# Kernel tuning notes

Measured on AMD Instinct MI355X. Metric: run time of the kernel, lower is better.

Reference implementation:

```python
import jax, jax.numpy as jnp
import numpy as np

SQRT_QKV_DIM = 8.0  # sqrt(qkv_dim=64)


def setup_inputs() -> dict:
    key = jax.random.key(0)
    ks = jax.random.split(key, 8)
    B, H, T, M, d, hid = 4, 16, 512, 512, 64, 16
    return {
        "q": jax.random.normal(ks[0], (B, H, T, d), dtype=jnp.float32),
        "k": jax.random.normal(ks[1], (B, H, M, d), dtype=jnp.float32),
        "v": jax.random.normal(ks[2], (B, H, M, d), dtype=jnp.float32),
        "D_TM": jax.random.uniform(ks[3], (B, T, M), dtype=jnp.float32),
        "mix1_weight": jax.random.uniform(ks[4], (H, 2, hid), minval=-0.7071, maxval=0.7071, dtype=jnp.float32),
        "mix1_bias": jax.random.uniform(ks[5], (H, hid), minval=-0.7071, maxval=0.7071, dtype=jnp.float32),
        "mix2_weight": jax.random.uniform(ks[6], (H, hid, 1), minval=-0.25, maxval=0.25, dtype=jnp.float32),
        "mix2_bias": jax.random.uniform(ks[7], (H, 1), minval=-0.25, maxval=0.25, dtype=jnp.float32),
    }


def reference(q, k, v, D_TM, mix1_weight, mix1_bias, mix2_weight, mix2_bias):
    B, H, T, d = q.shape
    Mc = k.shape[2]
    # scaled dot-product score: (B,H,T,M)
    dot_score = jnp.einsum("bhtd,bhmd->bhtm", q, k) / SQRT_QKV_DIM
    # per-head 2->hidden->1 MLP mixing dot score and distance bias.
    # Avoid explicit stack: linear layer over the 2 score channels expands as
    # dot*W1[:,0,:] + D*W1[:,1,:].  ms1: (B,H,T,M,hid)
    w1_dot = mix1_weight[:, 0, :][None, :, None, None, :]   # (1,H,1,1,hid)
    w1_dist = mix1_weight[:, 1, :][None, :, None, None, :]
    ms1 = (dot_score[..., None] * w1_dot
           + D_TM[:, None, :, :, None] * w1_dist
           + mix1_bias[None, :, None, None, :])
    ms1 = jax.nn.relu(ms1)
    # hidden -> 1: mixed_scores (B,H,T,M)
    mixed = jnp.einsum("bhtmc,hc->bhtm", ms1, mix2_weight[:, :, 0])
    mixed = mixed + mix2_bias[:, 0][None, :, None, None]
    weights = jax.nn.softmax(mixed, axis=3)
    out = jnp.einsum("bhtm,bhmd->bhtd", weights, v)   # (B,H,T,d)
    return out.transpose(0, 2, 1, 3).reshape(B, T, H * d)
```

## Files before the change

### kernel.cpp

```cpp
#include <hip/hip_runtime.h>
#include <stdint.h>

typedef __attribute__((ext_vector_type(8))) short short8;
typedef __attribute__((ext_vector_type(4))) float floatx4;

#define MFMA(a, b, c) __builtin_amdgcn_mfma_f32_16x16x32_bf16(a, b, c, 0, 0, 0)

union Frag { uint32_t u[4]; short8 s; };

__device__ __forceinline__ void packsplit(float a, float b, uint32_t& hi, uint32_t& lo) {
    uint32_t ua = __float_as_uint(a), ub = __float_as_uint(b);
    uint32_t ha = ua & 0xFFFF0000u, hb = ub & 0xFFFF0000u;
    float ra = a - __uint_as_float(ha);
    float rb = b - __uint_as_float(hb);
    hi = (ha >> 16) | hb;
    lo = (__float_as_uint(ra) >> 16) | (__float_as_uint(rb) & 0xFFFF0000u);
}

#define KHI 0
#define KLO 4608
#define VTHI 0
#define VTLO 4352
#define PHI 8704
#define PLO 13056

__global__ __launch_bounds__(256, 2)
void msmha_mfma(const float* __restrict__ qg, const float* __restrict__ kg,
                const float* __restrict__ vg, const float* __restrict__ Dg,
                const float* __restrict__ m1w, const float* __restrict__ m1b,
                const float* __restrict__ m2w, const float* __restrict__ m2b,
                float* __restrict__ outg) {
    __shared__ __align__(16) uint32_t sm[17408];
    __shared__ __align__(16) float wlds[68];

    const int tid  = threadIdx.x;
    const int w    = tid >> 6;
    const int lane = tid & 63;
    const int col  = lane & 15;
    const int quad = lane >> 4;

    const int bid = blockIdx.x;
    const int wgT = bid & 7;
    const int bh  = bid >> 3;
    const int h   = bh & 15;
    const int b   = bh >> 4;
    const int t0g = wgT * 64;

    const size_t base = (size_t)bh * 512 * 64;

    if (tid < 16) {
        wlds[4 * tid + 0] = m1w[h * 32 + tid];
        wlds[4 * tid + 1] = m1w[h * 32 + 16 + tid];
        wlds[4 * tid + 2] = m1b[h * 16 + tid];
        wlds[4 * tid + 3] = m2w[h * 16 + tid];
    }
    if (tid == 16) wlds[64] = m2b[h];

    Frag qh[2], ql[2];
    {
        const float* qrow = qg + base + (size_t)(t0g + w * 16 + col) * 64;
#pragma unroll
        for (int ks = 0; ks < 2; ++ks) {
            const float4 f0 = *(const float4*)(qrow + ks * 32 + quad * 8);
            const float4 f1 = *(const float4*)(qrow + ks * 32 + quad * 8 + 4);
            packsplit(f0.x, f0.y, qh[ks].u[0], ql[ks].u[0]);
            packsplit(f0.z, f0.w, qh[ks].u[1], ql[ks].u[1]);
            packsplit(f1.x, f1.y, qh[ks].u[2], ql[ks].u[2]);
            packsplit(f1.z, f1.w, qh[ks].u[3], ql[ks].u[3]);
        }
    }

    floatx4 accA[32];

    const float* Dbase = Dg + ((size_t)b * 512 + t0g + w * 16 + col) * 512 + quad * 4;

#pragma unroll
    for (int mc = 0; mc < 4; ++mc) {
        __syncthreads();
#pragma unroll
        for (int it = 0; it < 8; ++it) {
            const int i  = tid + it * 256;
            const int ml = i >> 4, k4 = i & 15;
            const float4 f = *(const float4*)(kg + base + (size_t)(mc * 128 + ml) * 64 + k4 * 4);
            uint32_t h0, l0, h1, l1;
            packsplit(f.x, f.y, h0, l0);
            packsplit(f.z, f.w, h1, l1);
            *(uint2*)(sm + KHI + ml * 36 + 2 * k4) = make_uint2(h0, h1);
            *(uint2*)(sm + KLO + ml * 36 + 2 * k4) = make_uint2(l0, l1);
        }
        __syncthreads();

        float4 dv[8];
#pragma unroll
        for (int mt = 0; mt < 8; ++mt)
            dv[mt] = *(const float4*)(Dbase + mc * 128 + mt * 16);

#pragma unroll
        for (int mt = 0; mt < 8; ++mt) {
            floatx4 acc = {0.f, 0.f, 0.f, 0.f};
#pragma unroll
            for (int ks = 0; ks < 2; ++ks) {
                const int ro = (mt * 16 + col) * 36 + 16 * ks + 4 * quad;
                Frag ah, al;
                ah.s = *(short8*)(sm + KHI + ro);
                al.s = *(short8*)(sm + KLO + ro);
                acc = MFMA(ah.s, qh[ks].s, acc);
                acc = MFMA(ah.s, ql[ks].s, acc);
                acc = MFMA(al.s, qh[ks].s, acc);
            }
            accA[mc * 8 + mt] = acc;
        }

        float mix[32];
        const float b2v = wlds[64];
#pragma unroll
        for (int mt = 0; mt < 8; ++mt)
#pragma unroll
            for (int r = 0; r < 4; ++r) {
                accA[mc * 8 + mt][r] *= 0.125f;
                mix[mt * 4 + r] = b2v;
            }
#pragma unroll 1
        for (int c = 0; c < 16; ++c) {
            const float4 wv = *(const float4*)(wlds + 4 * c);
#pragma unroll
            for (int mt = 0; mt < 8; ++mt) {
                const float4 dd = dv[mt];
                const float dr[4] = {dd.x, dd.y, dd.z, dd.w};
#pragma unroll
                for (int r = 0; r < 4; ++r) {
                    const float hh = fmaf(accA[mc * 8 + mt][r], wv.x, fmaf(dr[r], wv.y, wv.z));
                    mix[mt * 4 + r] = fmaf(fmaxf(hh, 0.f), wv.w, mix[mt * 4 + r]);
                }
            }
        }
#pragma unroll
        for (int mt = 0; mt < 8; ++mt)
#pragma unroll
            for (int r = 0; r < 4; ++r)
                accA[mc * 8 + mt][r] = mix[mt * 4 + r];
    }

    float mx = -3.4e38f;
#pragma unroll
    for (int i = 0; i < 32; ++i)
#pragma unroll
        for (int r = 0; r < 4; ++r) mx = fmaxf(mx, accA[i][r]);
    mx = fmaxf(mx, __shfl_xor(mx, 16, 64));
    mx = fmaxf(mx, __shfl_xor(mx, 32, 64));
    float sum = 0.f;
#pragma unroll
    for (int i = 0; i < 32; ++i)
#pragma unroll
        for (int r = 0; r < 4; ++r) {
            const float e = __expf(accA[i][r] - mx);
            accA[i][r] = e;
            sum += e;
        }
    sum += __shfl_xor(sum, 16, 64);
    sum += __shfl_xor(sum, 32, 64);
    const float rinv = 1.f / sum;
#pragma unroll
    for (int i = 0; i < 32; ++i)
#pragma unroll
        for (int r = 0; r < 4; ++r) accA[i][r] *= rinv;

    floatx4 oacc[4];
#pragma unroll
    for (int dt = 0; dt < 4; ++dt) oacc[dt] = floatx4{0.f, 0.f, 0.f, 0.f};

#pragma unroll
    for (int mc = 0; mc < 4; ++mc) {
        __syncthreads();
#pragma unroll
        for (int it = 0; it < 4; ++it) {
            const int u  = tid + it * 256;
            const int d4 = u & 15, m2 = u >> 4;
            const float4 f0 = *(const float4*)(vg + base + (size_t)(mc * 128 + 2 * m2) * 64 + d4 * 4);
            const float4 f1 = *(const float4*)(vg + base + (size_t)(mc * 128 + 2 * m2 + 1) * 64 + d4 * 4);
            const float a0[4] = {f0.x, f0.y, f0.z, f0.w};
            const float a1[4] = {f1.x, f1.y, f1.z, f1.w};
#pragma unroll
            for (int i = 0; i < 4; ++i) {
                uint32_t hw, lw;
                packsplit(a0[i], a1[i], hw, lw);
                sm[VTHI + (d4 * 4 + i) * 68 + m2] = hw;
                sm[VTLO + (d4 * 4 + i) * 68 + m2] = lw;
            }
        }
        {
            const int prow = (w * 16 + col) * 68;
#pragma unroll
            for (int mt = 0; mt < 8; ++mt) {
                const floatx4 pv = accA[mc * 8 + mt];
                uint32_t h0, l0, h1, l1;
                packsplit(pv[0], pv[1], h0, l0);
                packsplit(pv[2], pv[3], h1, l1);
                *(uint2*)(sm + PHI + prow + mt * 8 + 2 * quad) = make_uint2(h0, h1);
                *(uint2*)(sm + PLO + prow + mt * 8 + 2 * quad) = make_uint2(l0, l1);
            }
        }
        __syncthreads();
#pragma unroll
        for (int ks = 0; ks < 4; ++ks) {
            const int po = (w * 16 + col) * 68 + 16 * ks + 4 * quad;
            Frag pah, pal;
            pah.s = *(short8*)(sm + PHI + po);
            pal.s = *(short8*)(sm + PLO + po);
#pragma unroll
            for (int dt = 0; dt < 4; ++dt) {
                const int vo = (dt * 16 + col) * 68 + 16 * ks + 4 * quad;
                Frag bh, bl;
                bh.s = *(short8*)(sm + VTHI + vo);
                bl.s = *(short8*)(sm + VTLO + vo);
                oacc[dt] = MFMA(pah.s, bh.s, oacc[dt]);
                oacc[dt] = MFMA(pah.s, bl.s, oacc[dt]);
                oacc[dt] = MFMA(pal.s, bh.s, oacc[dt]);
            }
        }
    }

    const size_t obase = ((size_t)b * 512 + t0g + w * 16 + quad * 4) * 1024 + h * 64 + col;
#pragma unroll
    for (int dt = 0; dt < 4; ++dt)
#pragma unroll
        for (int r = 0; r < 4; ++r)
            outg[obase + (size_t)r * 1024 + dt * 16] = oacc[dt][r];
}

extern "C" void kernel_launch(void* const* d_in, const int* in_sizes, int n_in,
                              void* d_out, int out_size, void* d_ws, size_t ws_size,
                              hipStream_t stream) {
    const float* q   = (const float*)d_in[0];
    const float* k   = (const float*)d_in[1];
    const float* v   = (const float*)d_in[2];
    const float* dtm = (const float*)d_in[3];
    const float* m1w = (const float*)d_in[4];
    const float* m1b = (const float*)d_in[5];
    const float* m2w = (const float*)d_in[6];
    const float* m2b = (const float*)d_in[7];
    float* out = (float*)d_out;

    dim3 grid(4 * 16 * 8);
    dim3 block(256);
    msmha_mfma<<<grid, block, 0, stream>>>(q, k, v, dtm, m1w, m1b, m2w, m2b, out);
}
```

Before: 132.6 us.

## Double-buffer K/V loads, pack MLP with v_pk_fma, shuffle P fragments

Rewrites the kernel around 64-row K and V chunks held in double-buffered LDS, prefetching the next chunk into registers while computing the current one. The per-element MLP now runs on packed two-wide f32 FMAs. The P operand for the PV MFMA is rearranged with lane shuffles instead of a round trip through LDS. Smaller changes: the 1/8 scale is folded into Q, bf16 splitting now uses round-to-nearest, and a fourth lo*lo MFMA is added to QK. These cut LDS footprint and barrier stalls at the cost of extra shuffles, extra MFMAs and more synchronisation points.

```diff
diff --git a/kernel.cpp b/kernel.cpp
--- a/kernel.cpp
+++ b/kernel.cpp
@@ -1,231 +1,296 @@
 #include <hip/hip_runtime.h>
 #include <stdint.h>
 
+typedef __attribute__((ext_vector_type(2))) float fx2;
+typedef __attribute__((ext_vector_type(4))) float fx4;
 typedef __attribute__((ext_vector_type(8))) short short8;
-typedef __attribute__((ext_vector_type(4))) float floatx4;
-
-#define MFMA(a, b, c) __builtin_amdgcn_mfma_f32_16x16x32_bf16(a, b, c, 0, 0, 0)
+
+#define MFMA(a,b,c) __builtin_amdgcn_mfma_f32_16x16x32_bf16(a,b,c,0,0,0)
 
 union Frag { uint32_t u[4]; short8 s; };
 
+__device__ __forceinline__ uint32_t bf16rne(float x) {
+    uint32_t u = __float_as_uint(x);
+    return (u + 0x7FFFu + ((u >> 16) & 1u)) & 0xFFFF0000u;
+}
+
 __device__ __forceinline__ void packsplit(float a, float b, uint32_t& hi, uint32_t& lo) {
-    uint32_t ua = __float_as_uint(a), ub = __float_as_uint(b);
-    uint32_t ha = ua & 0xFFFF0000u, hb = ub & 0xFFFF0000u;
+    uint32_t ha = bf16rne(a), hb = bf16rne(b);
     float ra = a - __uint_as_float(ha);
     float rb = b - __uint_as_float(hb);
-    hi = (ha >> 16) | hb;
-    lo = (__float_as_uint(ra) >> 16) | (__float_as_uint(rb) & 0xFFFF0000u);
-}
-
-#define KHI 0
-#define KLO 4608
-#define VTHI 0
-#define VTLO 4352
-#define PHI 8704
-#define PLO 13056
+    hi = (ha >> 16) | (hb & 0xFFFF0000u);
+    lo = (bf16rne(ra) >> 16) | (bf16rne(rb) & 0xFFFF0000u);
+}
+
+__device__ __forceinline__ fx2 pkfma_bLO(fx2 a, fx2 b, fx2 c) {
+    fx2 d; asm("v_pk_fma_f32 %0, %1, %2, %3 op_sel:[0,0,0] op_sel_hi:[1,0,1]"
+               : "=v"(d) : "v"(a), "v"(b), "v"(c)); return d;
+}
+__device__ __forceinline__ fx2 pkfma_bHI(fx2 a, fx2 b, fx2 c) {
+    fx2 d; asm("v_pk_fma_f32 %0, %1, %2, %3 op_sel:[0,1,0] op_sel_hi:[1,1,1]"
+               : "=v"(d) : "v"(a), "v"(b), "v"(c)); return d;
+}
+__device__ __forceinline__ fx2 pkfma_bHI_cLO(fx2 a, fx2 b, fx2 c) {
+    fx2 d; asm("v_pk_fma_f32 %0, %1, %2, %3 op_sel:[0,1,0] op_sel_hi:[1,1,0]"
+               : "=v"(d) : "v"(a), "v"(b), "v"(c)); return d;
+}
 
 __global__ __launch_bounds__(256, 2)
-void msmha_mfma(const float* __restrict__ qg, const float* __restrict__ kg,
-                const float* __restrict__ vg, const float* __restrict__ Dg,
-                const float* __restrict__ m1w, const float* __restrict__ m1b,
-                const float* __restrict__ m2w, const float* __restrict__ m2b,
-                float* __restrict__ outg) {
-    __shared__ __align__(16) uint32_t sm[17408];
-    __shared__ __align__(16) float wlds[68];
+void msmha_v5(const float* __restrict__ qg, const float* __restrict__ kg,
+              const float* __restrict__ vg, const float* __restrict__ Dg,
+              const float* __restrict__ m1w, const float* __restrict__ m1b,
+              const float* __restrict__ m2w, const float* __restrict__ m2b,
+              float* __restrict__ outg) {
+    __shared__ __align__(16) uint32_t sm[9284];
+    float* smF = (float*)sm;
 
     const int tid  = threadIdx.x;
-    const int w    = tid >> 6;
-    const int lane = tid & 63;
-    const int col  = lane & 15;
-    const int quad = lane >> 4;
-
-    const int bid = blockIdx.x;
-    const int wgT = bid & 7;
-    const int bh  = bid >> 3;
-    const int h   = bh & 15;
-    const int b   = bh >> 4;
-    const int t0g = wgT * 64;
+    const int w    = tid >> 6, lane = tid & 63;
+    const int col  = lane & 15, Q = lane >> 4;
+
+    const int bid  = blockIdx.x;
+    const int tile = bid & 7, bh = bid >> 3;
+    const int h    = bh & 15, b = bh >> 4;
+    const int t0g  = tile * 64;
 
     const size_t base = (size_t)bh * 512 * 64;
 
     if (tid < 16) {
-        wlds[4 * tid + 0] = m1w[h * 32 + tid];
-        wlds[4 * tid + 1] = m1w[h * 32 + 16 + tid];
-        wlds[4 * tid + 2] = m1b[h * 16 + tid];
-        wlds[4 * tid + 3] = m2w[h * 16 + tid];
-    }
-    if (tid == 16) wlds[64] = m2b[h];
-
+        smF[9216 + 4*tid + 0] = m1w[h*32 + tid];
+        smF[9216 + 4*tid + 1] = m1w[h*32 + 16 + tid];
+        smF[9216 + 4*tid + 2] = m1b[h*16 + tid];
+        smF[9216 + 4*tid + 3] = m2w[h*16 + tid];
+    }
+    const float b2v = m2b[h];
+
+    const int trow = t0g + w*16 + col;
     Frag qh[2], ql[2];
     {
-        const float* qrow = qg + base + (size_t)(t0g + w * 16 + col) * 64;
+        const float* qr = qg + base + (size_t)trow * 64;
 #pragma unroll
         for (int ks = 0; ks < 2; ++ks) {
-            const float4 f0 = *(const float4*)(qrow + ks * 32 + quad * 8);
-            const float4 f1 = *(const float4*)(qrow + ks * 32 + quad * 8 + 4);
+            fx4 f0 = *(const fx4*)(qr + ks*32 + Q*8);
+            fx4 f1 = *(const fx4*)(qr + ks*32 + Q*8 + 4);
+            f0 *= 0.125f; f1 *= 0.125f;
             packsplit(f0.x, f0.y, qh[ks].u[0], ql[ks].u[0]);
             packsplit(f0.z, f0.w, qh[ks].u[1], ql[ks].u[1]);
             packsplit(f1.x, f1.y, qh[ks].u[2], ql[ks].u[2]);
             packsplit(f1.z, f1.w, qh[ks].u[3], ql[ks].u[3]);
         }
     }
-
-    floatx4 accA[32];
-
-    const float* Dbase = Dg + ((size_t)b * 512 + t0g + w * 16 + col) * 512 + quad * 4;
-
-#pragma unroll
-    for (int mc = 0; mc < 4; ++mc) {
-        __syncthreads();
-#pragma unroll
-        for (int it = 0; it < 8; ++it) {
-            const int i  = tid + it * 256;
-            const int ml = i >> 4, k4 = i & 15;
-            const float4 f = *(const float4*)(kg + base + (size_t)(mc * 128 + ml) * 64 + k4 * 4);
-            uint32_t h0, l0, h1, l1;
-            packsplit(f.x, f.y, h0, l0);
-            packsplit(f.z, f.w, h1, l1);
-            *(uint2*)(sm + KHI + ml * 36 + 2 * k4) = make_uint2(h0, h1);
-            *(uint2*)(sm + KLO + ml * 36 + 2 * k4) = make_uint2(l0, l1);
-        }
-        __syncthreads();
-
-        float4 dv[8];
-#pragma unroll
-        for (int mt = 0; mt < 8; ++mt)
-            dv[mt] = *(const float4*)(Dbase + mc * 128 + mt * 16);
-
-#pragma unroll
-        for (int mt = 0; mt < 8; ++mt) {
-            floatx4 acc = {0.f, 0.f, 0.f, 0.f};
+    const float* Drow = Dg + ((size_t)b*512 + trow) * 512;
+
+    fx4 accA[32];
+    fx4 oacc[4] = {};
+
+    const int k4 = tid & 15, mrow = tid >> 4;
+    const int vm2 = tid & 31, vd4 = tid >> 5;
+
+    {
+        fx4 kreg[4];
+#pragma unroll
+        for (int it = 0; it < 4; ++it)
+            kreg[it] = *(const fx4*)(kg + base + (size_t)(mrow + 16*it)*64 + 4*k4);
+#pragma unroll
+        for (int it = 0; it < 4; ++it) {
+            uint32_t h0,l0,h1,l1;
+            packsplit(kreg[it].x, kreg[it].y, h0, l0);
+            packsplit(kreg[it].z, kreg[it].w, h1, l1);
+            const int ro = (mrow + 16*it)*36 + 2*k4;
+            *(uint2*)(sm + ro)        = make_uint2(h0,h1);
+            *(uint2*)(sm + 2304 + ro) = make_uint2(l0,l1);
+        }
+    }
+    __syncthreads();
+
+#pragma unroll 1
+    for (int c = 0; c < 8; ++c) {
+        const int cur = (c & 1) * 4608;
+        fx4 knext[4];
+        if (c < 7) {
+#pragma unroll
+            for (int it = 0; it < 4; ++it)
+                knext[it] = *(const fx4*)(kg + base + (size_t)((c+1)*64 + mrow + 16*it)*64 + 4*k4);
+        }
+        fx4 dv[4];
+#pragma unroll
+        for (int mt = 0; mt < 4; ++mt)
+            dv[mt] = *(const fx4*)(Drow + c*64 + mt*16 + 4*Q);
+
+#pragma unroll
+        for (int mt = 0; mt < 4; ++mt) {
+            fx4 acc = {};
 #pragma unroll
             for (int ks = 0; ks < 2; ++ks) {
-                const int ro = (mt * 16 + col) * 36 + 16 * ks + 4 * quad;
+                const int ro = cur + (mt*16 + col)*36 + ks*16 + 4*Q;
                 Frag ah, al;
-                ah.s = *(short8*)(sm + KHI + ro);
-                al.s = *(short8*)(sm + KLO + ro);
+                ah.s = *(short8*)(sm + ro);
+                al.s = *(short8*)(sm + 2304 + ro);
                 acc = MFMA(ah.s, qh[ks].s, acc);
                 acc = MFMA(ah.s, ql[ks].s, acc);
                 acc = MFMA(al.s, qh[ks].s, acc);
-            }
-            accA[mc * 8 + mt] = acc;
-        }
-
-        float mix[32];
-        const float b2v = wlds[64];
-#pragma unroll
-        for (int mt = 0; mt < 8; ++mt)
+                acc = MFMA(al.s, ql[ks].s, acc);
+            }
+            accA[c*4 + mt] = acc;
+        }
+
+        fx2 S2[8], D2[8], mix[8];
+#pragma unroll
+        for (int mt = 0; mt < 4; ++mt) {
+            S2[2*mt]   = fx2{accA[c*4+mt].x, accA[c*4+mt].y};
+            S2[2*mt+1] = fx2{accA[c*4+mt].z, accA[c*4+mt].w};
+            D2[2*mt]   = fx2{dv[mt].x, dv[mt].y};
+            D2[2*mt+1] = fx2{dv[mt].z, dv[mt].w};
+            mix[2*mt]  = fx2{b2v, b2v};
+            mix[2*mt+1]= fx2{b2v, b2v};
+        }
+#pragma unroll 1
+        for (int cc = 0; cc < 16; ++cc) {
+            fx2 w01 = *(const fx2*)(smF + 9216 + 4*cc);
+            fx2 w23 = *(const fx2*)(smF + 9216 + 4*cc + 2);
+#pragma unroll
+            for (int p = 0; p < 8; ++p) {
+                fx2 dt_ = pkfma_bHI_cLO(D2[p], w01, w23);
+                fx2 hh  = pkfma_bLO(S2[p], w01, dt_);
+                fx2 rr  = { fmaxf(hh.x, 0.f), fmaxf(hh.y, 0.f) };
+                mix[p]  = pkfma_bHI(rr, w23, mix[p]);
+            }
+        }
+#pragma unroll
+        for (int mt = 0; mt < 4; ++mt)
+            accA[c*4+mt] = fx4{mix[2*mt].x, mix[2*mt].y, mix[2*mt+1].x, mix[2*mt+1].y};
+
+        if (c < 7) {
+            const int nxt = 4608 - cur;
+#pragma unroll
+            for (int it = 0; it < 4; ++it) {
+                uint32_t h0,l0,h1,l1;
+                packsplit(knext[it].x, knext[it].y, h0, l0);
+                packsplit(knext[it].z, knext[it].w, h1, l1);
+                const int ro = (mrow + 16*it)*36 + 2*k4;
+                *(uint2*)(sm + nxt + ro)        = make_uint2(h0,h1);
+                *(uint2*)(sm + nxt + 2304 + ro) = make_uint2(l0,l1);
+            }
+        }
+        __syncthreads();
+    }
+
+    fx4 vreg[2][2];
+#pragma unroll
+    for (int it = 0; it < 2; ++it) {
+        const float* vr = vg + base + (size_t)(2*vm2)*64 + 4*(vd4 + 8*it);
+        vreg[it][0] = *(const fx4*)vr;
+        vreg[it][1] = *(const fx4*)(vr + 64);
+    }
+
+    {
+        float mx = -3.0e38f;
+#pragma unroll
+        for (int i = 0; i < 32; ++i)
+#pragma unroll
+            for (int r = 0; r < 4; ++r) mx = fmaxf(mx, accA[i][r]);
+        mx = fmaxf(mx, __shfl_xor(mx, 16, 64));
+        mx = fmaxf(mx, __shfl_xor(mx, 32, 64));
+        float sum = 0.f;
+#pragma unroll
+        for (int i = 0; i < 32; ++i)
 #pragma unroll
             for (int r = 0; r < 4; ++r) {
-                accA[mc * 8 + mt][r] *= 0.125f;
-                mix[mt * 4 + r] = b2v;
-            }
+                const float e = __expf(accA[i][r] - mx);
+                accA[i][r] = e;
+                sum += e;
+            }
+        sum += __shfl_xor(sum, 16, 64);
+        sum += __shfl_xor(sum, 32, 64);
+        const float rinv = 1.f / sum;
+#pragma unroll
+        for (int i = 0; i < 32; ++i)
+#pragma unroll
+            for (int r = 0; r < 4; ++r) accA[i][r] *= rinv;
+    }
+
+#pragma unroll
+    for (int it = 0; it < 2; ++it) {
+        const int d4 = vd4 + 8*it;
+#pragma unroll
+        for (int i = 0; i < 4; ++i) {
+            uint32_t hw, lw;
+            packsplit(vreg[it][0][i], vreg[it][1][i], hw, lw);
+            sm[(4*d4 + i)*36 + vm2]        = hw;
+            sm[2304 + (4*d4 + i)*36 + vm2] = lw;
+        }
+    }
+    __syncthreads();
+
+    const int sbase = col | ((lane & 16) << 1);
 #pragma unroll 1
-        for (int c = 0; c < 16; ++c) {
-            const float4 wv = *(const float4*)(wlds + 4 * c);
-#pragma unroll
-            for (int mt = 0; mt < 8; ++mt) {
-                const float4 dd = dv[mt];
-                const float dr[4] = {dd.x, dd.y, dd.z, dd.w};
-#pragma unroll
-                for (int r = 0; r < 4; ++r) {
-                    const float hh = fmaf(accA[mc * 8 + mt][r], wv.x, fmaf(dr[r], wv.y, wv.z));
-                    mix[mt * 4 + r] = fmaf(fmaxf(hh, 0.f), wv.w, mix[mt * 4 + r]);
+    for (int c = 0; c < 8; ++c) {
+        const int cur = (c & 1) * 4608;
+        fx4 vnext[2][2];
+        if (c < 7) {
+#pragma unroll
+            for (int it = 0; it < 2; ++it) {
+                const float* vr = vg + base + (size_t)((c+1)*64 + 2*vm2)*64 + 4*(vd4 + 8*it);
+                vnext[it][0] = *(const fx4*)vr;
+                vnext[it][1] = *(const fx4*)(vr + 64);
+            }
+        }
+#pragma unroll
+        for (int s = 0; s < 2; ++s) {
+            const fx4 e0 = accA[c*4 + 2*s], e1 = accA[c*4 + 2*s + 1];
+            uint32_t ph[4], pl[4];
+            packsplit(e0.x, e0.y, ph[0], pl[0]);
+            packsplit(e0.z, e0.w, ph[1], pl[1]);
+            packsplit(e1.x, e1.y, ph[2], pl[2]);
+            packsplit(e1.z, e1.w, ph[3], pl[3]);
+            Frag Ah, Al;
+#pragma unroll
+            for (int dd = 0; dd < 4; ++dd) {
+                const int sl = sbase + ((dd >> 1) << 4);
+                const int pi = dd & 1;
+                uint32_t h0 = (uint32_t)__shfl((int)ph[pi],   sl, 64);
+                uint32_t h1 = (uint32_t)__shfl((int)ph[2+pi], sl, 64);
+                uint32_t l0 = (uint32_t)__shfl((int)pl[pi],   sl, 64);
+                uint32_t l1 = (uint32_t)__shfl((int)pl[2+pi], sl, 64);
+                Ah.u[dd] = (lane & 32) ? h1 : h0;
+                Al.u[dd] = (lane & 32) ? l1 : l0;
+            }
+#pragma unroll
+            for (int dt = 0; dt < 4; ++dt) {
+                const int vo = cur + (dt*16 + col)*36 + s*16 + 4*Q;
+                Frag bh_, bl_;
+                bh_.s = *(short8*)(sm + vo);
+                bl_.s = *(short8*)(sm + vo + 2304);
+                oacc[dt] = MFMA(Ah.s, bh_.s, oacc[dt]);
+                oacc[dt] = MFMA(Ah.s, bl_.s, oacc[dt]);
+                oacc[dt] = MFMA(Al.s, bh_.s, oacc[dt]);
+            }
+        }
+        if (c < 7) {
+            const int nxt = 4608 - cur;
+#pragma unroll
+            for (int it = 0; it < 2; ++it) {
+                const int d4 = vd4 + 8*it;
+#pragma unroll
+                for (int i = 0; i < 4; ++i) {
+                    uint32_t hw, lw;
+                    packsplit(vnext[it][0][i], vnext[it][1][i], hw, lw);
+                    sm[nxt + (4*d4 + i)*36 + vm2]        = hw;
+                    sm[nxt + 2304 + (4*d4 + i)*36 + vm2] = lw;
                 }
             }
         }
-#pragma unroll
-        for (int mt = 0; mt < 8; ++mt)
-#pragma unroll
-            for (int r = 0; r < 4; ++r)
-                accA[mc * 8 + mt][r] = mix[mt * 4 + r];
-    }
-
-    float mx = -3.4e38f;
-#pragma unroll
-    for (int i = 0; i < 32; ++i)
-#pragma unroll
-        for (int r = 0; r < 4; ++r) mx = fmaxf(mx, accA[i][r]);
-    mx = fmaxf(mx, __shfl_xor(mx, 16, 64));
-    mx = fmaxf(mx, __shfl_xor(mx, 32, 64));
-    float sum = 0.f;
-#pragma unroll
-    for (int i = 0; i < 32; ++i)
-#pragma unroll
-        for (int r = 0; r < 4; ++r) {
-            const float e = __expf(accA[i][r] - mx);
-            accA[i][r] = e;
-            sum += e;
-        }
-    sum += __shfl_xor(sum, 16, 64);
-    sum += __shfl_xor(sum, 32, 64);
-    const float rinv = 1.f / sum;
-#pragma unroll
-    for (int i = 0; i < 32; ++i)
-#pragma unroll
-        for (int r = 0; r < 4; ++r) accA[i][r] *= rinv;
-
-    floatx4 oacc[4];
-#pragma unroll
-    for (int dt = 0; dt < 4; ++dt) oacc[dt] = floatx4{0.f, 0.f, 0.f, 0.f};
-
-#pragma unroll
-    for (int mc = 0; mc < 4; ++mc) {
         __syncthreads();
-#pragma unroll
-        for (int it = 0; it < 4; ++it) {
-            const int u  = tid + it * 256;
-            const int d4 = u & 15, m2 = u >> 4;
-            const float4 f0 = *(const float4*)(vg + base + (size_t)(mc * 128 + 2 * m2) * 64 + d4 * 4);
-            const float4 f1 = *(const float4*)(vg + base + (size_t)(mc * 128 + 2 * m2 + 1) * 64 + d4 * 4);
-            const float a0[4] = {f0.x, f0.y, f0.z, f0.w};
-            const float a1[4] = {f1.x, f1.y, f1.z, f1.w};
-#pragma unroll
-            for (int i = 0; i < 4; ++i) {
-                uint32_t hw, lw;
-                packsplit(a0[i], a1[i], hw, lw);
-                sm[VTHI + (d4 * 4 + i) * 68 + m2] = hw;
-                sm[VTLO + (d4 * 4 + i) * 68 + m2] = lw;
-            }
-        }
-        {
-            const int prow = (w * 16 + col) * 68;
-#pragma unroll
-            for (int mt = 0; mt < 8; ++mt) {
-                const floatx4 pv = accA[mc * 8 + mt];
-                uint32_t h0, l0, h1, l1;
-                packsplit(pv[0], pv[1], h0, l0);
-                packsplit(pv[2], pv[3], h1, l1);
-                *(uint2*)(sm + PHI + prow + mt * 8 + 2 * quad) = make_uint2(h0, h1);
-                *(uint2*)(sm + PLO + prow + mt * 8 + 2 * quad) = make_uint2(l0, l1);
-            }
-        }
-        __syncthreads();
-#pragma unroll
-        for (int ks = 0; ks < 4; ++ks) {
-            const int po = (w * 16 + col) * 68 + 16 * ks + 4 * quad;
-            Frag pah, pal;
-            pah.s = *(short8*)(sm + PHI + po);
-            pal.s = *(short8*)(sm + PLO + po);
-#pragma unroll
-            for (int dt = 0; dt < 4; ++dt) {
-                const int vo = (dt * 16 + col) * 68 + 16 * ks + 4 * quad;
-                Frag bh, bl;
-                bh.s = *(short8*)(sm + VTHI + vo);
-                bl.s = *(short8*)(sm + VTLO + vo);
-                oacc[dt] = MFMA(pah.s, bh.s, oacc[dt]);
-                oacc[dt] = MFMA(pah.s, bl.s, oacc[dt]);
-                oacc[dt] = MFMA(pal.s, bh.s, oacc[dt]);
-            }
-        }
-    }
-
-    const size_t obase = ((size_t)b * 512 + t0g + w * 16 + quad * 4) * 1024 + h * 64 + col;
-#pragma unroll
-    for (int dt = 0; dt < 4; ++dt)
+    }
+
+    const size_t ob = ((size_t)b*512 + t0g + w*16 + 4*Q)*1024 + h*64 + col;
+#pragma unroll
+    for (int dt = 0; dt < 4; ++dt) {
+        const fx4 o4 = oacc[dt];
 #pragma unroll
         for (int r = 0; r < 4; ++r)
-            outg[obase + (size_t)r * 1024 + dt * 16] = oacc[dt][r];
+            outg[ob + (size_t)r*1024 + dt*16] = o4[r];
+    }
 }
 
 extern "C" void kernel_launch(void* const* d_in, const int* in_sizes, int n_in,
@@ -241,7 +306,7 @@
     const float* m2b = (const float*)d_in[7];
     float* out = (float*)d_out;
 
-    dim3 grid(4 * 16 * 8);
+    dim3 grid(64 * 8);
     dim3 block(256);
-    msmha_mfma<<<grid, block, 0, stream>>>(q, k, v, dtm, m1w, m1b, m2w, m2b, out);
-}
+    msmha_v5<<<grid, block, 0, stream>>>(q, k, v, dtm, m1w, m1b, m2w, m2b, out);
+}
```

Result: slower. 200.8 us (+51.5%).
